# Kernel optimization log

Measured on AMD Instinct MI355X. Metric: run time of the kernel, lower is better.

## Reference

```python
import jax, jax.numpy as jnp
import numpy as np

B, D, NS, C, H = 4096, 1024, 16000, 1000, 256


def setup_inputs() -> dict:
    key = jax.random.key(0)
    ks = jax.random.split(key, 8)
    # L2-normalized image features (output of frozen CLIP encode_image + norm)
    q = jax.random.normal(ks[0], (B, D), jnp.float32)
    q = q / jnp.linalg.norm(q, axis=-1, keepdims=True)
    # zero-shot CLIP logits
    z = jax.random.normal(ks[1], (B, C), jnp.float32)
    # L2-normalized support/cache features
    keys = jax.random.normal(ks[2], (NS, D), jnp.float32)
    keys = keys / jnp.linalg.norm(keys, axis=-1, keepdims=True)
    # one-hot support labels
    labels = jax.random.randint(ks[3], (NS,), 0, C)
    values = jax.nn.one_hot(labels, C, dtype=jnp.float32)
    # gate MLP params (small init like nn.Linear default scale)
    fc1_w = jax.random.normal(ks[4], (H, D), jnp.float32) * 0.02
    fc1_b = jnp.zeros((H,), jnp.float32)
    fc2_w = jax.random.normal(ks[5], (2, H), jnp.float32) * 0.02
    fc2_b = jnp.zeros((2,), jnp.float32)
    post_scale = jnp.ones((1,), jnp.float32)
    return {"q": q, "z": z, "keys": keys, "values": values,
            "fc1_w": fc1_w, "fc1_b": fc1_b, "fc2_w": fc2_w, "fc2_b": fc2_b,
            "post_scale": post_scale}


def reference(q, z, keys, values, fc1_w, fc1_b, fc2_w, fc2_b, post_scale):
    # GateMLP: per-image alpha in (0,1), beta > 0
    x = jax.nn.relu(q @ fc1_w.T + fc1_b)            # [B, H]
    g = x @ fc2_w.T + fc2_b                          # [B, 2]
    alpha_hat = jax.nn.sigmoid(g[:, 0:1])            # [B, 1]
    beta = jax.nn.softplus(g[:, 1:2]) + 0.001        # [B, 1] (learn_beta=True)
    # cache logits: sim -> exp affinity -> label aggregation
    sim = q @ keys.T                                 # [B, Ns]
    affinity = jnp.exp(beta * sim)                   # [B, Ns]
    c = affinity @ values                            # [B, C]
    # gated convex fusion with zero-shot logits
    logits = ((1.0 - alpha_hat) * z + alpha_hat * c) * post_scale
    return (logits, alpha_hat, beta)
```

## Files before the change

kernel.cpp:

```cpp
#include <hip/hip_runtime.h>
#include <hip/hip_bf16.h>
#include <stdint.h>

#define B_  4096
#define D_  1024
#define NS_ 16000
#define C_  1000
#define H_  256
#define LBLK 4000

typedef __attribute__((ext_vector_type(8))) short bf16x8;
typedef __attribute__((ext_vector_type(4))) float f32x4;
typedef __attribute__((ext_vector_type(16))) float f32x16;
typedef __attribute__((ext_vector_type(8))) int i32x8;

__device__ __forceinline__ unsigned short f2bf(float f) {
  union { float f; unsigned u; } v; v.f = f;
  unsigned u = v.u;
  u += 0x7FFF + ((u >> 16) & 1);
  return (unsigned short)(u >> 16);
}

__device__ __forceinline__ float bf2f(unsigned short h) {
  union { unsigned u; float f; } v; v.u = ((unsigned)h) << 16;
  return v.f;
}

__global__ void prep_kernel(const float4* __restrict__ q, const float4* __restrict__ keys,
                            const float4* __restrict__ fc1, const float* __restrict__ values,
                            ushort4* __restrict__ qb, int* __restrict__ q8,
                            int* __restrict__ keys8, ushort4* __restrict__ fc1b,
                            int* __restrict__ labels, int* __restrict__ hist) {
  if (blockIdx.x < LBLK) {
    const int s = blockIdx.x * 4 + (threadIdx.x >> 6);
    const int lane = threadIdx.x & 63;
    const float4* row = (const float4*)(values + (size_t)s * C_);
    int lab = -1;
    for (int j = lane; j < C_ / 4; j += 64) {
      float4 v = row[j];
      if (v.x > 0.5f) lab = j * 4 + 0;
      if (v.y > 0.5f) lab = j * 4 + 1;
      if (v.z > 0.5f) lab = j * 4 + 2;
      if (v.w > 0.5f) lab = j * 4 + 3;
      if (__ballot(lab >= 0)) break;
    }
    if (lab >= 0) { labels[s] = lab; atomicAdd(&hist[lab], 1); }
    return;
  }
  const size_t nq = (size_t)B_ * D_ / 4;
  const size_t nk = (size_t)NS_ * D_ / 4;
  const size_t nf = (size_t)H_ * D_ / 4;
  const size_t total = nq + nk + nf;
  const size_t nblk = gridDim.x - LBLK;
  for (size_t i = (blockIdx.x - LBLK) * (size_t)blockDim.x + threadIdx.x; i < total;
       i += nblk * blockDim.x) {
    if (i < nq) {
      float4 v = q[i];
      ushort4 r; r.x = f2bf(v.x); r.y = f2bf(v.y); r.z = f2bf(v.z); r.w = f2bf(v.w);
      qb[i] = r;
      int p = __builtin_amdgcn_cvt_pk_fp8_f32(v.x * 64.f, v.y * 64.f, 0, false);
      p     = __builtin_amdgcn_cvt_pk_fp8_f32(v.z * 64.f, v.w * 64.f, p, true);
      q8[i] = p;
    } else if (i < nq + nk) {
      size_t o = i - nq;
      float4 v = keys[o];
      int p = __builtin_amdgcn_cvt_pk_fp8_f32(v.x * 64.f, v.y * 64.f, 0, false);
      p     = __builtin_amdgcn_cvt_pk_fp8_f32(v.z * 64.f, v.w * 64.f, p, true);
      keys8[o] = p;
    } else {
      size_t o = i - nq - nk;
      float4 v = fc1[o];
      ushort4 r; r.x = f2bf(v.x); r.y = f2bf(v.y); r.z = f2bf(v.z); r.w = f2bf(v.w);
      fc1b[o] = r;
    }
  }
}

__global__ void scan_kernel(const int* __restrict__ hist, int* __restrict__ boff) {
  __shared__ int s[1024];
  const int t = threadIdx.x;
  int v = (t < C_) ? hist[t] : 0;
  s[t] = v; __syncthreads();
  for (int off = 1; off < 1024; off <<= 1) {
    int u = (t >= off) ? s[t - off] : 0;
    __syncthreads();
    s[t] += u;
    __syncthreads();
  }
  if (t == 0) boff[0] = 0;
  if (t < C_) boff[t + 1] = s[t];
}

__global__ void scatter_kernel(const int* __restrict__ labels, const int* __restrict__ boff,
                               int* __restrict__ cnt, int* __restrict__ sortidx) {
  const int sidx = blockIdx.x * blockDim.x + threadIdx.x;
  if (sidx >= NS_) return;
  const int lab = labels[sidx];
  const int pos = boff[lab] + atomicAdd(&cnt[lab], 1);
  sortidx[pos] = sidx;
}

template<int MODE>
__global__ __launch_bounds__(256, 2) void gemm_kernel(
    const short* __restrict__ A, const short* __restrict__ Bm,
    const float* __restrict__ bias, float* __restrict__ outp)
{
  __shared__ short As[128 * 64];
  __shared__ short Bs[128 * 64];

  const int tid  = threadIdx.x;
  const int wave = tid >> 6, lane = tid & 63;
  const int quad = lane >> 4, l16 = lane & 15;
  const int wm = wave >> 1, wn = wave & 1;
  const int rstart = blockIdx.x * 128;
  const int nstart = blockIdx.y * 128;

  f32x4 acc[4][4];
  #pragma unroll
  for (int i = 0; i < 4; ++i)
    #pragma unroll
    for (int j = 0; j < 4; ++j) acc[i][j] = (f32x4)0.f;

  const int r_  = (lane >> 3);
  const int kc_ = ((lane & 7) ^ r_) * 8;

  for (int kt = 0; kt < D_; kt += 64) {
    __syncthreads();
    #pragma unroll
    for (int i = 0; i < 4; ++i) {
      const int chunk = i * 4 + wave;
      const int r = chunk * 8 + r_;
      const short* gA = A  + (size_t)(rstart + r) * D_ + kt + kc_;
      const short* gB = Bm + (size_t)(nstart + r) * D_ + kt + kc_;
      __builtin_amdgcn_global_load_lds(
          (const __attribute__((address_space(1))) void*)gA,
          (__attribute__((address_space(3))) void*)(As + chunk * 512), 16, 0, 0);
      __builtin_amdgcn_global_load_lds(
          (const __attribute__((address_space(1))) void*)gB,
          (__attribute__((address_space(3))) void*)(Bs + chunk * 512), 16, 0, 0);
    }
    __syncthreads();
    #pragma unroll
    for (int ks = 0; ks < 64; ks += 32) {
      bf16x8 af[4], bfr[4];
      const int kb = (ks >> 3) + quad;
      #pragma unroll
      for (int mt = 0; mt < 4; ++mt) {
        const int row = wm * 64 + mt * 16 + l16;
        af[mt] = *(const bf16x8*)(As + row * 64 + ((kb ^ (row & 7)) << 3));
      }
      #pragma unroll
      for (int nt = 0; nt < 4; ++nt) {
        const int row = wn * 64 + nt * 16 + l16;
        bfr[nt] = *(const bf16x8*)(Bs + row * 64 + ((kb ^ (row & 7)) << 3));
      }
      #pragma unroll
      for (int mt = 0; mt < 4; ++mt)
        #pragma unroll
        for (int nt = 0; nt < 4; ++nt)
          acc[mt][nt] = __builtin_amdgcn_mfma_f32_16x16x32_bf16(af[mt], bfr[nt], acc[mt][nt], 0, 0, 0);
    }
  }

  #pragma unroll
  for (int mt = 0; mt < 4; ++mt) {
    const int rbase = wm * 64 + mt * 16 + quad * 4;
    #pragma unroll
    for (int nt = 0; nt < 4; ++nt) {
      const int cc = nstart + wn * 64 + nt * 16 + l16;
      const float bv = bias[cc];
      #pragma unroll
      for (int r = 0; r < 4; ++r) {
        float v = acc[mt][nt][r] + bv;
        outp[(size_t)(rstart + rbase + r) * H_ + cc] = v > 0.f ? v : 0.f;
      }
    }
  }
}

__device__ __forceinline__ i32x8 mx_frag(const char* base, int lrow, int kh, int sel) {
  const int c0 = kh * 4 + sel * 2;
  const int s = lrow & 7;
  const int4 lo = *(const int4*)(base + lrow * 128 + (((c0    ) ^ s) << 4));
  const int4 hi = *(const int4*)(base + lrow * 128 + (((c0 + 1) ^ s) << 4));
  i32x8 f;
  f[0] = lo.x; f[1] = lo.y; f[2] = lo.z; f[3] = lo.w;
  f[4] = hi.x; f[5] = hi.y; f[6] = hi.z; f[7] = hi.w;
  return f;
}

__global__ __launch_bounds__(256, 2) void mxgemm_kernel(
    const char* __restrict__ A8, const char* __restrict__ B8,
    const float* __restrict__ beta, unsigned short* __restrict__ affbuf,
    long affStride, const int* __restrict__ sortidx)
{
  __shared__ char As[128 * 128];
  __shared__ char Bs[128 * 128];
  __shared__ float sbeta[128];

  const int tid  = threadIdx.x;
  const int wave = tid >> 6, lane = tid & 63;
  const int sel  = lane >> 5, l32 = lane & 31;
  const int wm = wave >> 1, wn = wave & 1;
  const int rstart = blockIdx.x * 128;
  const int nstart = blockIdx.y * 128;

  if (tid < 128) sbeta[tid] = beta[rstart + tid];

  const int srow_ = (lane >> 3);
  const int gch_  = (lane & 7) ^ srow_;

  int arow[4], brow[4];
  #pragma unroll
  for (int i = 0; i < 4; ++i) {
    const int row = wave * 32 + i * 8 + srow_;
    arow[i] = rstart + row;
    brow[i] = sortidx[nstart + row];
  }

  f32x16 acc[2][2];
  #pragma unroll
  for (int i = 0; i < 2; ++i)
    #pragma unroll
    for (int j = 0; j < 2; ++j) acc[i][j] = (f32x16)0.f;

  for (int kt = 0; kt < D_; kt += 128) {
    __syncthreads();
    #pragma unroll
    for (int i = 0; i < 4; ++i) {
      const char* gA = A8 + (size_t)arow[i] * D_ + kt + (gch_ << 4);
      const char* gB = B8 + (size_t)brow[i] * D_ + kt + (gch_ << 4);
      __builtin_amdgcn_global_load_lds(
          (const __attribute__((address_space(1))) void*)gA,
          (__attribute__((address_space(3))) void*)(As + wave * 4096 + i * 1024), 16, 0, 0);
      __builtin_amdgcn_global_load_lds(
          (const __attribute__((address_space(1))) void*)gB,
          (__attribute__((address_space(3))) void*)(Bs + wave * 4096 + i * 1024), 16, 0, 0);
    }
    __syncthreads();
    #pragma unroll
    for (int kh = 0; kh < 2; ++kh) {
      i32x8 a0 = mx_frag(As, wm * 64 +  0 + l32, kh, sel);
      i32x8 a1 = mx_frag(As, wm * 64 + 32 + l32, kh, sel);
      i32x8 b0 = mx_frag(Bs, wn * 64 +  0 + l32, kh, sel);
      i32x8 b1 = mx_frag(Bs, wn * 64 + 32 + l32, kh, sel);
      acc[0][0] = __builtin_amdgcn_mfma_scale_f32_32x32x64_f8f6f4(a0, b0, acc[0][0], 0, 0, 0, 121, 0, 121);
      acc[0][1] = __builtin_amdgcn_mfma_scale_f32_32x32x64_f8f6f4(a0, b1, acc[0][1], 0, 0, 0, 121, 0, 121);
      acc[1][0] = __builtin_amdgcn_mfma_scale_f32_32x32x64_f8f6f4(a1, b0, acc[1][0], 0, 0, 0, 121, 0, 121);
      acc[1][1] = __builtin_amdgcn_mfma_scale_f32_32x32x64_f8f6f4(a1, b1, acc[1][1], 0, 0, 0, 121, 0, 121);
    }
  }

  #pragma unroll
  for (int mt = 0; mt < 2; ++mt) {
    #pragma unroll
    for (int nt = 0; nt < 2; ++nt) {
      const long col = nstart + wn * 64 + nt * 32 + l32;
      #pragma unroll
      for (int r = 0; r < 16; ++r) {
        const int row = wm * 64 + mt * 32 + (r & 3) + 8 * (r >> 2) + 4 * sel;
        const float v = __expf(sbeta[row] * acc[mt][nt][r]);
        affbuf[(size_t)(rstart + row) * affStride + col] = f2bf(v);
      }
    }
  }
}

__global__ void gate_kernel(const float* __restrict__ x, const float* __restrict__ fc2_w,
                            const float* __restrict__ fc2_b, float* __restrict__ ab) {
  const int w = (int)((blockIdx.x * blockDim.x + threadIdx.x) >> 6);
  const int lane = threadIdx.x & 63;
  if (w >= B_) return;
  const float* xr = x + (size_t)w * H_;
  float g0 = 0.f, g1 = 0.f;
  #pragma unroll
  for (int j = 0; j < H_; j += 64) {
    float v = xr[j + lane];
    g0 += v * fc2_w[j + lane];
    g1 += v * fc2_w[H_ + j + lane];
  }
  #pragma unroll
  for (int off = 32; off > 0; off >>= 1) {
    g0 += __shfl_down(g0, off);
    g1 += __shfl_down(g1, off);
  }
  if (lane == 0) {
    g0 += fc2_b[0];
    g1 += fc2_b[1];
    ab[w]      = 1.f / (1.f + __expf(-g0));
    ab[B_ + w] = fmaxf(g1, 0.f) + log1pf(__expf(-fabsf(g1))) + 0.001f;
  }
}

__global__ __launch_bounds__(256) void segsum_kernel(
    const unsigned short* __restrict__ aff, const int* __restrict__ boff,
    float* __restrict__ out, const float* __restrict__ z, const float* __restrict__ ps,
    int n0, int n1, long affStride, int flags) {
  __shared__ unsigned short srow[16384];
  __shared__ int sboff[C_ + 1];
  const int b = blockIdx.x;
  const int t = threadIdx.x;
  const int nc = n1 - n0;
  const int4* src = (const int4*)(aff + (size_t)b * affStride);
  int4* dst = (int4*)srow;
  for (int i = t; i < nc / 8; i += 256) dst[i] = src[i];
  for (int i = t; i <= C_; i += 256) sboff[i] = boff[i];
  __syncthreads();
  float a = 0.f, sc = 1.f;
  if (flags & 2) { a = out[(size_t)B_ * C_ + b]; sc = ps[0]; }
  for (int lab = t; lab < C_; lab += 256) {
    int s0 = sboff[lab], s1 = sboff[lab + 1];
    if (s0 < n0) s0 = n0;
    if (s1 > n1) s1 = n1;
    float sum = 0.f;
    for (int s = s0; s < s1; ++s) sum += bf2f(srow[s - n0]);
    const size_t oi = (size_t)b * C_ + lab;
    float c = (flags & 1) ? sum : out[oi] + sum;
    out[oi] = (flags & 2) ? ((1.f - a) * z[oi] + a * c) * sc : c;
  }
}

extern "C" void kernel_launch(void* const* d_in, const int* in_sizes, int n_in,
                              void* d_out, int out_size, void* d_ws, size_t ws_size,
                              hipStream_t stream) {
  const float* q          = (const float*)d_in[0];
  const float* z          = (const float*)d_in[1];
  const float* keys       = (const float*)d_in[2];
  const float* values     = (const float*)d_in[3];
  const float* fc1_w      = (const float*)d_in[4];
  const float* fc1_b      = (const float*)d_in[5];
  const float* fc2_w      = (const float*)d_in[6];
  const float* fc2_b      = (const float*)d_in[7];
  const float* post_scale = (const float*)d_in[8];
  float* out = (float*)d_out;

  char* ws = (char*)d_ws;
  short*          qb      = (short*)(ws);
  char*           q8      = (char*) (ws +  8388608);
  char*           keys8   = (char*) (ws + 12582912);
  short*          fc1b    = (short*)(ws + 28966912);
  int*            labels  = (int*)  (ws + 29491200);
  float*          x       = (float*)(ws + 29555200);
  int*            hist    = (int*)  (ws + 33749504);
  int*            cnt     = (int*)  (ws + 33753600);
  int*            boff    = (int*)  (ws + 33757696);
  int*            sortidx = (int*)  (ws + 33761792);
  unsigned short* aff     = (unsigned short*)(ws + 33825792);

  float* alpha = out + (size_t)B_ * C_;
  float* beta  = alpha + B_;

  long avail = (long)ws_size - 33825792L;
  long maxN = (avail / (B_ * 2)) & ~127L;
  if (maxN > NS_) maxN = NS_;
  if (maxN > 16384) maxN = 16384;
  if (maxN < 128) maxN = 128;

  hipMemsetAsync(hist, 0, 8192, stream);

  prep_kernel<<<LBLK + 2048, 256, 0, stream>>>(
      (const float4*)q, (const float4*)keys, (const float4*)fc1_w, values,
      (ushort4*)qb, (int*)q8, (int*)keys8, (ushort4*)fc1b, labels, hist);

  scan_kernel<<<1, 1024, 0, stream>>>(hist, boff);
  scatter_kernel<<<(NS_ + 255) / 256, 256, 0, stream>>>(labels, boff, cnt, sortidx);

  gemm_kernel<1><<<dim3(B_ / 128, H_ / 128), 256, 0, stream>>>(qb, fc1b, fc1_b, x);

  gate_kernel<<<(B_ * 64) / 256, 256, 0, stream>>>(x, fc2_w, fc2_b, alpha);

  for (long n0 = 0; n0 < NS_; n0 += maxN) {
    long nc = NS_ - n0; if (nc > maxN) nc = maxN;
    mxgemm_kernel<<<dim3(B_ / 128, (int)(nc / 128)), 256, 0, stream>>>(
        q8, keys8, beta, aff, maxN, sortidx + n0);
    int flags = (n0 == 0 ? 1 : 0) | ((n0 + nc >= NS_) ? 2 : 0);
    segsum_kernel<<<B_, 256, 0, stream>>>(aff, boff, out, z, post_scale,
                                          (int)n0, (int)(n0 + nc), maxN, flags);
  }
}
```

Baseline: 338.6 us.

## Fuse label segment-sum into MX GEMM epilogue with atomic accumulation

```diff
diff --git a/kernel.cpp b/kernel.cpp
--- a/kernel.cpp
+++ b/kernel.cpp
@@ -92,12 +92,14 @@
 }
 
 __global__ void scatter_kernel(const int* __restrict__ labels, const int* __restrict__ boff,
-                               int* __restrict__ cnt, int* __restrict__ sortidx) {
+                               int* __restrict__ cnt, int* __restrict__ sortidx,
+                               int* __restrict__ labsorted) {
   const int sidx = blockIdx.x * blockDim.x + threadIdx.x;
   if (sidx >= NS_) return;
   const int lab = labels[sidx];
   const int pos = boff[lab] + atomicAdd(&cnt[lab], 1);
   sortidx[pos] = sidx;
+  labsorted[pos] = lab;
 }
 
 template<int MODE>
@@ -191,21 +193,28 @@
 
 __global__ __launch_bounds__(256, 2) void mxgemm_kernel(
     const char* __restrict__ A8, const char* __restrict__ B8,
-    const float* __restrict__ beta, unsigned short* __restrict__ affbuf,
-    long affStride, const int* __restrict__ sortidx)
+    const float* __restrict__ beta, float* __restrict__ out,
+    const int* __restrict__ sortidx, const int* __restrict__ labsorted)
 {
-  __shared__ char As[128 * 128];
-  __shared__ char Bs[128 * 128];
+  __shared__ char smem[32768];
   __shared__ float sbeta[128];
+  __shared__ int slab[128];
+  char* As = smem;
+  char* Bs = smem + 16384;
 
   const int tid  = threadIdx.x;
   const int wave = tid >> 6, lane = tid & 63;
   const int sel  = lane >> 5, l32 = lane & 31;
   const int wm = wave >> 1, wn = wave & 1;
-  const int rstart = blockIdx.x * 128;
-  const int nstart = blockIdx.y * 128;
-
-  if (tid < 128) sbeta[tid] = beta[rstart + tid];
+
+  const int sb  = (blockIdx.x & 7) * 500 + (blockIdx.x >> 3);
+  const int rstart = (sb & 31) * 128;
+  const int nstart = (sb >> 5) * 128;
+
+  if (tid < 128) {
+    sbeta[tid] = beta[rstart + tid];
+    slab[tid]  = labsorted[nstart + tid];
+  }
 
   const int srow_ = (lane >> 3);
   const int gch_  = (lane & 7) ^ srow_;
@@ -251,19 +260,36 @@
     }
   }
 
+  __syncthreads();
+  unsigned short* tile = (unsigned short*)smem;
   #pragma unroll
   for (int mt = 0; mt < 2; ++mt) {
     #pragma unroll
     for (int nt = 0; nt < 2; ++nt) {
-      const long col = nstart + wn * 64 + nt * 32 + l32;
+      const int col = wn * 64 + nt * 32 + l32;
       #pragma unroll
       for (int r = 0; r < 16; ++r) {
         const int row = wm * 64 + mt * 32 + (r & 3) + 8 * (r >> 2) + 4 * sel;
         const float v = __expf(sbeta[row] * acc[mt][nt][r]);
-        affbuf[(size_t)(rstart + row) * affStride + col] = f2bf(v);
+        tile[row * 128 + (col ^ (row & 63) ^ ((row & 4) << 3))] = f2bf(v);
       }
     }
   }
+  __syncthreads();
+
+  const int row = tid & 127;
+  const int c0  = (tid >> 7) * 64;
+  const int rxm = (row & 63) ^ ((row & 4) << 3);
+  const unsigned short* trow = tile + row * 128;
+  float* orow = out + (size_t)(rstart + row) * C_;
+  int lab = slab[c0];
+  float sum = 0.f;
+  for (int c = c0; c < c0 + 64; ++c) {
+    const int l = slab[c];
+    if (l != lab) { atomicAdd(orow + lab, sum); sum = 0.f; lab = l; }
+    sum += bf2f(trow[c ^ rxm]);
+  }
+  atomicAdd(orow + lab, sum);
 }
 
 __global__ void gate_kernel(const float* __restrict__ x, const float* __restrict__ fc2_w,
@@ -292,32 +318,22 @@
   }
 }
 
-__global__ __launch_bounds__(256) void segsum_kernel(
-    const unsigned short* __restrict__ aff, const int* __restrict__ boff,
-    float* __restrict__ out, const float* __restrict__ z, const float* __restrict__ ps,
-    int n0, int n1, long affStride, int flags) {
-  __shared__ unsigned short srow[16384];
-  __shared__ int sboff[C_ + 1];
+__global__ __launch_bounds__(256) void fuse_kernel(float* __restrict__ out,
+                                                   const float* __restrict__ z,
+                                                   const float* __restrict__ ps) {
   const int b = blockIdx.x;
   const int t = threadIdx.x;
-  const int nc = n1 - n0;
-  const int4* src = (const int4*)(aff + (size_t)b * affStride);
-  int4* dst = (int4*)srow;
-  for (int i = t; i < nc / 8; i += 256) dst[i] = src[i];
-  for (int i = t; i <= C_; i += 256) sboff[i] = boff[i];
-  __syncthreads();
-  float a = 0.f, sc = 1.f;
-  if (flags & 2) { a = out[(size_t)B_ * C_ + b]; sc = ps[0]; }
-  for (int lab = t; lab < C_; lab += 256) {
-    int s0 = sboff[lab], s1 = sboff[lab + 1];
-    if (s0 < n0) s0 = n0;
-    if (s1 > n1) s1 = n1;
-    float sum = 0.f;
-    for (int s = s0; s < s1; ++s) sum += bf2f(srow[s - n0]);
-    const size_t oi = (size_t)b * C_ + lab;
-    float c = (flags & 1) ? sum : out[oi] + sum;
-    out[oi] = (flags & 2) ? ((1.f - a) * z[oi] + a * c) * sc : c;
-  }
+  if (t >= C_ / 4) return;
+  const float a  = out[(size_t)B_ * C_ + b];
+  const float sc = ps[0];
+  float4* o4 = (float4*)(out + (size_t)b * C_);
+  const float4* z4 = (const float4*)(z + (size_t)b * C_);
+  float4 c = o4[t], zz = z4[t], r;
+  r.x = ((1.f - a) * zz.x + a * c.x) * sc;
+  r.y = ((1.f - a) * zz.y + a * c.y) * sc;
+  r.z = ((1.f - a) * zz.z + a * c.z) * sc;
+  r.w = ((1.f - a) * zz.w + a * c.w) * sc;
+  o4[t] = r;
 }
 
 extern "C" void kernel_launch(void* const* d_in, const int* in_sizes, int n_in,
@@ -335,46 +351,38 @@
   float* out = (float*)d_out;
 
   char* ws = (char*)d_ws;
-  short*          qb      = (short*)(ws);
-  char*           q8      = (char*) (ws +  8388608);
-  char*           keys8   = (char*) (ws + 12582912);
-  short*          fc1b    = (short*)(ws + 28966912);
-  int*            labels  = (int*)  (ws + 29491200);
-  float*          x       = (float*)(ws + 29555200);
-  int*            hist    = (int*)  (ws + 33749504);
-  int*            cnt     = (int*)  (ws + 33753600);
-  int*            boff    = (int*)  (ws + 33757696);
-  int*            sortidx = (int*)  (ws + 33761792);
-  unsigned short* aff     = (unsigned short*)(ws + 33825792);
+  short* qb        = (short*)(ws);
+  char*  q8        = (char*) (ws +  8388608);
+  char*  keys8     = (char*) (ws + 12582912);
+  short* fc1b      = (short*)(ws + 28966912);
+  int*   labels    = (int*)  (ws + 29491200);
+  float* x         = (float*)(ws + 29555200);
+  int*   hist      = (int*)  (ws + 33749504);
+  int*   cnt       = (int*)  (ws + 33753600);
+  int*   boff      = (int*)  (ws + 33757696);
+  int*   sortidx   = (int*)  (ws + 33761792);
+  int*   labsorted = (int*)  (ws + 33825792);
 
   float* alpha = out + (size_t)B_ * C_;
   float* beta  = alpha + B_;
 
-  long avail = (long)ws_size - 33825792L;
-  long maxN = (avail / (B_ * 2)) & ~127L;
-  if (maxN > NS_) maxN = NS_;
-  if (maxN > 16384) maxN = 16384;
-  if (maxN < 128) maxN = 128;
-
   hipMemsetAsync(hist, 0, 8192, stream);
+  hipMemsetAsync(out, 0, (size_t)B_ * C_ * sizeof(float), stream);
 
   prep_kernel<<<LBLK + 2048, 256, 0, stream>>>(
       (const float4*)q, (const float4*)keys, (const float4*)fc1_w, values,
       (ushort4*)qb, (int*)q8, (int*)keys8, (ushort4*)fc1b, labels, hist);
 
   scan_kernel<<<1, 1024, 0, stream>>>(hist, boff);
-  scatter_kernel<<<(NS_ + 255) / 256, 256, 0, stream>>>(labels, boff, cnt, sortidx);
+  scatter_kernel<<<(NS_ + 255) / 256, 256, 0, stream>>>(labels, boff, cnt, sortidx,
+                                                        labsorted);
 
   gemm_kernel<1><<<dim3(B_ / 128, H_ / 128), 256, 0, stream>>>(qb, fc1b, fc1_b, x);
 
   gate_kernel<<<(B_ * 64) / 256, 256, 0, stream>>>(x, fc2_w, fc2_b, alpha);
 
-  for (long n0 = 0; n0 < NS_; n0 += maxN) {
-    long nc = NS_ - n0; if (nc > maxN) nc = maxN;
-    mxgemm_kernel<<<dim3(B_ / 128, (int)(nc / 128)), 256, 0, stream>>>(
-        q8, keys8, beta, aff, maxN, sortidx + n0);
-    int flags = (n0 == 0 ? 1 : 0) | ((n0 + nc >= NS_) ? 2 : 0);
-    segsum_kernel<<<B_, 256, 0, stream>>>(aff, boff, out, z, post_scale,
-                                          (int)n0, (int)(n0 + nc), maxN, flags);
-  }
-}
+  mxgemm_kernel<<<(B_ / 128) * (NS_ / 128), 256, 0, stream>>>(
+      q8, keys8, beta, out, sortidx, labsorted);
+
+  fuse_kernel<<<B_, 256, 0, stream>>>(out, z, post_scale);
+}
```

Measured after the change: 541.3 us. +59.9%, slower.
